# Kernel tuning notes

Hardware: AMD Instinct MI355X
Metric: run time of the kernel (lower is better)

The kernel has to match this reference:

```python
import jax, jax.numpy as jnp
import numpy as np

B, F, D, H = 16384, 39, 16, 2   # batch, fields, embed_dim, heads
VOCAB = 10000                    # per-field vocab
DH = D * H                       # attention output dim per layer (no head split)


def setup_inputs() -> dict:
    key = jax.random.key(0)
    ks = jax.random.split(key, 32)
    def n(k, shape, s=0.05):
        return jax.random.normal(k, shape, jnp.float32) * s
    inp = {"x": jax.random.randint(ks[0], (B, F), 0, VOCAB, dtype=jnp.int32)}
    inp["emb"] = n(ks[1], (F * VOCAB, D))
    idx = 2
    for i, din in enumerate([D, DH, DH]):  # layer0: 16->32, layers 1-2: 32->32
        for nm in ["wq", "wk", "wv", "wr"]:
            inp[f"{nm}{i}"] = n(ks[idx], (din, DH)); idx += 1
    prev = F * DH  # 1248 after flatten
    for i, u in enumerate([128, 64, 32, 1], 1):
        inp[f"w{i}"] = n(ks[idx], (prev, u)); idx += 1
        inp[f"b{i}"] = jnp.zeros((u,), jnp.float32)
        prev = u
    return inp


def reference(x, emb,
              wq0, wk0, wv0, wr0,
              wq1, wk1, wv1, wr1,
              wq2, wk2, wv2, wr2,
              w1, b1, w2, b2, w3, b3, w4, b4):
    offsets = jnp.arange(F, dtype=jnp.int32) * VOCAB
    e = emb[x + offsets]                                   # [B, F, D]
    for wq, wk, wv, wr in [(wq0, wk0, wv0, wr0),
                           (wq1, wk1, wv1, wr1),
                           (wq2, wk2, wv2, wr2)]:
        q = jnp.einsum('bfd,de->bfe', e, wq)               # [B, F, DH]
        k = jnp.einsum('bfd,de->bfe', e, wk)
        v = jnp.einsum('bfd,de->bfe', e, wv)
        att = jax.nn.softmax(jnp.einsum('bfe,bge->bfg', q, k), axis=-1)  # [B,F,F], no scaling
        out = jnp.einsum('bfg,bge->bfe', att, v) + jnp.einsum('bfd,de->bfe', e, wr)
        e = jax.nn.relu(out)
    h = e.reshape(B, F * DH)
    for w, b in [(w1, b1), (w2, b2), (w3, b3)]:
        h = jax.nn.relu(h @ w + b)
    return jax.nn.sigmoid(h @ w4 + b4)                     # [B, 1]
```

## Files before the change

kernel.cpp:

```cpp
#include <hip/hip_runtime.h>
#include <math.h>

#define NF   39
#define NB   16384
#define NVOC 10000

typedef unsigned short u16;
typedef unsigned int   u32;
typedef float f32x4 __attribute__((ext_vector_type(4)));
typedef short s16x8 __attribute__((ext_vector_type(8)));

#define E3_U16   20447232u
#define NSWZ     182272

__device__ __forceinline__ u32 bfadj(float x){
    u32 u = __float_as_uint(x);
    return u + 0x7fffu + ((u >> 16) & 1u);
}
__device__ __forceinline__ u32 pk2(float a, float b){
    return __builtin_amdgcn_perm(bfadj(a), bfadj(b), 0x03020706u);
}
__device__ __forceinline__ u16 f2bf(float f){ return (u16)(bfadj(f) >> 16); }

__device__ __forceinline__ void wave_sync(){
    asm volatile("s_waitcnt lgkmcnt(0)" ::: "memory");
}
__device__ __forceinline__ f32x4 mfma16(s16x8 a, s16x8 b, f32x4 c){
    return __builtin_amdgcn_mfma_f32_16x16x32_bf16(a, b, c, 0, 0, 0);
}
__device__ __forceinline__ void store4(u16* p, f32x4 v){
    *(uint2*)p = make_uint2(pk2(v[0], v[1]), pk2(v[2], v[3]));
}

__global__ void __launch_bounds__(256) swz_kernel(
    const float* __restrict__ wq0, const float* __restrict__ wk0,
    const float* __restrict__ wv0, const float* __restrict__ wr0,
    const float* __restrict__ wq1, const float* __restrict__ wk1,
    const float* __restrict__ wv1, const float* __restrict__ wr1,
    const float* __restrict__ wq2, const float* __restrict__ wk2,
    const float* __restrict__ wv2, const float* __restrict__ wr2,
    const float* __restrict__ w1, const float* __restrict__ w2,
    const float* __restrict__ w3, u16* __restrict__ ws)
{
    int gid = (int)blockIdx.x*256 + (int)threadIdx.x;
    if (gid >= NSWZ) return;
    int w    = gid & 511;
    int lane = w >> 3, j = w & 7;
    int n    = lane & 15, quad = lane >> 4;
    int kin  = quad*8 + j;
    float val;
    if (gid < 12288){
        int mat = gid >> 10;
        int nt  = (gid >> 9) & 1;
        const float* W;
        switch (mat){
            case 0: W = wq0; break; case 1: W = wk0; break;
            case 2: W = wv0; break; case 3: W = wr0; break;
            case 4: W = wq1; break; case 5: W = wk1; break;
            case 6: W = wv1; break; case 7: W = wr1; break;
            case 8: W = wq2; break; case 9: W = wk2; break;
            case 10: W = wv2; break; default: W = wr2; break;
        }
        int din = (mat < 4) ? 16 : 32;
        val = (kin < din) ? W[kin*32 + nt*16 + n] : 0.f;
    } else if (gid < 12288 + 159744){
        int tt = (gid - 12288) >> 9;
        int ks = tt >> 3, nt = tt & 7;
        val = w1[(ks*32 + kin)*128 + nt*16 + n];
    } else if (gid < 12288 + 159744 + 8192){
        int tt = (gid - (12288+159744)) >> 9;
        int ks = tt >> 2, nt = tt & 3;
        val = w2[(ks*32 + kin)*64 + nt*16 + n];
    } else {
        int tt = (gid - (12288+159744+8192)) >> 9;
        int ks = tt >> 1, nt = tt & 1;
        val = w3[(ks*32 + kin)*32 + nt*16 + n];
    }
    ws[E3_U16 + gid] = f2bf(val);
}

__global__ void __launch_bounds__(256, 3) attn_kernel(
    const int* __restrict__ x, const float* __restrict__ emb,
    u16* __restrict__ ws)
{
    __shared__ __align__(16) u16 lds[4*6656];
    const int tid  = (int)threadIdx.x;
    const int wid  = tid >> 6, lane = tid & 63;
    const int h    = lane >> 4, nl = lane & 15;
    const int r    = (int)blockIdx.x*4 + wid;

    u16* eBuf = lds + wid*6656;
    u16* kBuf = eBuf + 1536;
    u16* qBuf = kBuf + 1536;
    u16* vBuf = qBuf + 1536;
    u16* pBuf = kBuf;
    const u16* wmat = ws + E3_U16;
    const f32x4 z = {0.f, 0.f, 0.f, 0.f};
    const int A_off = nl*8 + (h>>1)*128 + (h&1)*4;

    f32x4 ci;
#pragma unroll
    for (int reg = 0; reg < 4; ++reg)
        ci[reg] = (h*4 + reg >= 7) ? -1e30f : 0.f;

    if (lane < 48){
        int f = lane, mt = f >> 4, fl = f & 15;
        u16* row = eBuf + mt*512 + fl*8;
        if (f < NF){
            const float4* ep = (const float4*)(emb + ((size_t)(x[r*NF + f] + f*NVOC))*16);
            float4 e0 = ep[0], e1 = ep[1], e2 = ep[2], e3 = ep[3];
            *(uint4*)(row)       = make_uint4(pk2(e0.x,e0.y), pk2(e0.z,e0.w),
                                              pk2(e1.x,e1.y), pk2(e1.z,e1.w));
            *(uint4*)(row + 128) = make_uint4(pk2(e2.x,e2.y), pk2(e2.z,e2.w),
                                              pk2(e3.x,e3.y), pk2(e3.z,e3.w));
        } else {
            *(uint4*)(row)       = make_uint4(0,0,0,0);
            *(uint4*)(row + 128) = make_uint4(0,0,0,0);
        }
        *(uint4*)(row + 256) = make_uint4(0,0,0,0);
        *(uint4*)(row + 384) = make_uint4(0,0,0,0);
    }
    wave_sync();

#pragma unroll 1
    for (int L = 0; L < 3; ++L){
        const u16* wB = wmat + L*4096;
        s16x8 bE[3];
#pragma unroll
        for (int nt = 0; nt < 3; ++nt)
            bE[nt] = *(const s16x8*)(eBuf + nt*512 + lane*8);

        {
            s16x8 a0 = *(const s16x8*)(wB + lane*8);
            s16x8 a1 = *(const s16x8*)(wB + 512 + lane*8);
#pragma unroll
            for (int nt = 0; nt < 3; ++nt){
                store4(qBuf + nt*512       + A_off, mfma16(a0, bE[nt], z));
                store4(qBuf + nt*512 + 256 + A_off, mfma16(a1, bE[nt], z));
            }
        }
        {
            s16x8 a0 = *(const s16x8*)(wB + 1024 + lane*8);
            s16x8 a1 = *(const s16x8*)(wB + 1536 + lane*8);
#pragma unroll
            for (int nt = 0; nt < 3; ++nt){
                store4(kBuf + nt*512       + A_off, mfma16(a0, bE[nt], z));
                store4(kBuf + nt*512 + 256 + A_off, mfma16(a1, bE[nt], z));
            }
        }
        {
            s16x8 b0 = *(const s16x8*)(wB + 2048 + lane*8);
            s16x8 b1 = *(const s16x8*)(wB + 2560 + lane*8);
#pragma unroll
            for (int mtg = 0; mtg < 3; ++mtg){
                int toff = (mtg>>1)*1024 + (mtg&1)*256;
                store4(vBuf + toff       + A_off, mfma16(bE[mtg], b0, z));
                store4(vBuf + toff + 512 + A_off, mfma16(bE[mtg], b1, z));
            }
            *(uint2*)(vBuf + 2*512 + 256 + lane*4) = make_uint2(0,0);
            *(uint2*)(vBuf + 3*512 + 256 + lane*4) = make_uint2(0,0);
        }
        f32x4 R[2][3];
        {
            s16x8 a0 = *(const s16x8*)(wB + 3072 + lane*8);
            s16x8 a1 = *(const s16x8*)(wB + 3584 + lane*8);
#pragma unroll
            for (int nt = 0; nt < 3; ++nt){
                R[0][nt] = mfma16(a0, bE[nt], z);
                R[1][nt] = mfma16(a1, bE[nt], z);
            }
        }
        wave_sync();

        f32x4 S[3][3];
        {
            s16x8 aK[3], bQ[3];
#pragma unroll
            for (int i = 0; i < 3; ++i){
                aK[i] = *(const s16x8*)(kBuf + i*512 + lane*8);
                bQ[i] = *(const s16x8*)(qBuf + i*512 + lane*8);
            }
#pragma unroll
            for (int mtg = 0; mtg < 3; ++mtg)
#pragma unroll
            for (int nt = 0; nt < 3; ++nt)
                S[mtg][nt] = mfma16(aK[mtg], bQ[nt], (mtg == 2) ? ci : z);
        }
        float inv[3];
#pragma unroll
        for (int nt = 0; nt < 3; ++nt){
            float t = 0.f;
#pragma unroll
            for (int mtg = 0; mtg < 3; ++mtg)
#pragma unroll
            for (int reg = 0; reg < 4; ++reg){
                S[mtg][nt][reg] = __expf(S[mtg][nt][reg]);
                t += S[mtg][nt][reg];
            }
            t += __shfl_xor(t, 16, 64);
            t += __shfl_xor(t, 32, 64);
            inv[nt] = 1.0f / t;
        }
#pragma unroll
        for (int mtg = 0; mtg < 3; ++mtg)
#pragma unroll
        for (int nt = 0; nt < 3; ++nt){
            f32x4 p;
#pragma unroll
            for (int reg = 0; reg < 4; ++reg) p[reg] = S[mtg][nt][reg]*inv[nt];
            store4(pBuf + ((mtg>>1)*3 + nt)*512 + (mtg&1)*256 + A_off, p);
        }
        wave_sync();

        s16x8 aV[2][2], bP[2][3];
#pragma unroll
        for (int ks = 0; ks < 2; ++ks){
#pragma unroll
            for (int emt = 0; emt < 2; ++emt)
                aV[ks][emt] = *(const s16x8*)(vBuf + (ks*2+emt)*512 + lane*8);
#pragma unroll
            for (int nt = 0; nt < 3; ++nt)
                bP[ks][nt] = *(const s16x8*)(pBuf + (ks*3+nt)*512 + lane*8);
        }
        if (L < 2){
#pragma unroll
            for (int emt = 0; emt < 2; ++emt)
#pragma unroll
            for (int nt = 0; nt < 3; ++nt){
                f32x4 o = mfma16(aV[1][emt], bP[1][nt],
                         mfma16(aV[0][emt], bP[0][nt], z));
                float m = (nt < 2 || nl < 7) ? 1.f : 0.f;
#pragma unroll
                for (int reg = 0; reg < 4; ++reg)
                    o[reg] = fmaxf(o[reg] + R[emt][nt][reg], 0.f) * m;
                store4(eBuf + nt*512 + emt*256 + A_off, o);
            }
        } else {
            int st = r >> 4, sm = r & 15;
            u32 base = (u32)(st*39)*512u + (u32)(sm*8 + (h>>1)*128 + (h&1)*4);
#pragma unroll
            for (int emt = 0; emt < 2; ++emt)
#pragma unroll
            for (int nt = 0; nt < 3; ++nt){
                f32x4 o = mfma16(aV[1][emt], bP[1][nt],
                         mfma16(aV[0][emt], bP[0][nt], z));
#pragma unroll
                for (int reg = 0; reg < 4; ++reg)
                    o[reg] = fmaxf(o[reg] + R[emt][nt][reg], 0.f);
                int f = nt*16 + nl;
                if (f < NF)
                    *(uint2*)(ws + base + (u32)f*512u + emt*256) =
                        make_uint2(pk2(o[0], o[1]), pk2(o[2], o[3]));
            }
        }
        wave_sync();
    }
}

__global__ void __launch_bounds__(256, 4) mlp_kernel(
    const float* __restrict__ b1, const float* __restrict__ b2,
    const float* __restrict__ b3, const float* __restrict__ w4,
    const float* __restrict__ b4, const u16* __restrict__ ws,
    float* __restrict__ out)
{
    __shared__ __align__(16) u16 h1t[2048];
    __shared__ __align__(16) u16 h2t[1024];
    __shared__ float part[32];
    const int tid = (int)threadIdx.x;
    const int w   = tid >> 6, lane = tid & 63;
    const int h   = lane >> 4, nl = lane & 15;
    const int st  = (int)blockIdx.x;
    const int A_off = nl*8 + (h>>1)*128 + (h&1)*4;

    const u16* w1b = ws + E3_U16 + 12288u;
    const u16* w2b = w1b + 159744u;
    const u16* w3b = w2b + 8192u;
    const f32x4 z = {0.f,0.f,0.f,0.f};

    f32x4 acc[2] = {z, z};
#pragma unroll 2
    for (int ks = 0; ks < 39; ++ks){
        s16x8 aE = *(const s16x8*)(ws + (u32)(st*39 + ks)*512u + lane*8);
#pragma unroll
        for (int t = 0; t < 2; ++t){
            s16x8 aW = *(const s16x8*)(w1b + (ks*8 + 2*w + t)*512 + lane*8);
            acc[t] = mfma16(aW, aE, acc[t]);
        }
    }
#pragma unroll
    for (int t = 0; t < 2; ++t){
        float4 bv = *(const float4*)(b1 + (2*w + t)*16 + h*4);
        f32x4 v;
        v[0] = fmaxf(acc[t][0] + bv.x, 0.f);
        v[1] = fmaxf(acc[t][1] + bv.y, 0.f);
        v[2] = fmaxf(acc[t][2] + bv.z, 0.f);
        v[3] = fmaxf(acc[t][3] + bv.w, 0.f);
        store4(h1t + w*512 + t*256 + A_off, v);
    }
    __syncthreads();

    {
        f32x4 a2 = z;
#pragma unroll
        for (int ks = 0; ks < 4; ++ks){
            s16x8 aW = *(const s16x8*)(w2b + (ks*4 + w)*512 + lane*8);
            s16x8 bH = *(const s16x8*)(h1t + ks*512 + lane*8);
            a2 = mfma16(aW, bH, a2);
        }
        float4 bv = *(const float4*)(b2 + w*16 + h*4);
        f32x4 v;
        v[0] = fmaxf(a2[0] + bv.x, 0.f);
        v[1] = fmaxf(a2[1] + bv.y, 0.f);
        v[2] = fmaxf(a2[2] + bv.z, 0.f);
        v[3] = fmaxf(a2[3] + bv.w, 0.f);
        store4(h2t + (w>>1)*512 + (w&1)*256 + A_off, v);
    }
    __syncthreads();

    if (w < 2){
        f32x4 a3 = z;
#pragma unroll
        for (int ks = 0; ks < 2; ++ks){
            s16x8 aW = *(const s16x8*)(w3b + (ks*2 + w)*512 + lane*8);
            s16x8 bH = *(const s16x8*)(h2t + ks*512 + lane*8);
            a3 = mfma16(aW, bH, a3);
        }
        float4 b3v = *(const float4*)(b3 + w*16 + h*4);
        float4 w4v = *(const float4*)(w4 + w*16 + h*4);
        float t = fmaxf(a3[0] + b3v.x, 0.f)*w4v.x
                + fmaxf(a3[1] + b3v.y, 0.f)*w4v.y
                + fmaxf(a3[2] + b3v.z, 0.f)*w4v.z
                + fmaxf(a3[3] + b3v.w, 0.f)*w4v.w;
        t += __shfl_xor(t, 16, 64);
        t += __shfl_xor(t, 32, 64);
        if (h == 0) part[w*16 + nl] = t;
    }
    __syncthreads();
    if (tid < 16){
        float zz = part[tid] + part[16 + tid] + b4[0];
        out[st*16 + tid] = 1.f/(1.f + __expf(-zz));
    }
}

extern "C" void kernel_launch(void* const* d_in, const int* in_sizes, int n_in,
                              void* d_out, int out_size, void* d_ws, size_t ws_size,
                              hipStream_t stream)
{
    (void)in_sizes; (void)n_in; (void)ws_size; (void)out_size;
    const int*   x   = (const int*)d_in[0];
    const float* emb = (const float*)d_in[1];
    u16* ws = (u16*)d_ws;

    swz_kernel<<<(NSWZ+255)/256, 256, 0, stream>>>(
        (const float*)d_in[2],  (const float*)d_in[3],  (const float*)d_in[4],  (const float*)d_in[5],
        (const float*)d_in[6],  (const float*)d_in[7],  (const float*)d_in[8],  (const float*)d_in[9],
        (const float*)d_in[10], (const float*)d_in[11], (const float*)d_in[12], (const float*)d_in[13],
        (const float*)d_in[14], (const float*)d_in[16], (const float*)d_in[18], ws);

    attn_kernel<<<NB/4, 256, 0, stream>>>(x, emb, ws);

    mlp_kernel<<<NB/16, 256, 0, stream>>>(
        (const float*)d_in[15], (const float*)d_in[17], (const float*)d_in[19],
        (const float*)d_in[20], (const float*)d_in[21], ws, (float*)d_out);
}
```

Before: 195.3 us.

## Split MLP layer-1 K across waves, defer softmax normalization, use hardware bf16 pack

```diff
diff --git a/kernel.cpp b/kernel.cpp
--- a/kernel.cpp
+++ b/kernel.cpp
@@ -18,7 +18,12 @@
     return u + 0x7fffu + ((u >> 16) & 1u);
 }
 __device__ __forceinline__ u32 pk2(float a, float b){
+#if __has_builtin(__builtin_amdgcn_cvt_pk_bf16_f32)
+    auto t = __builtin_amdgcn_cvt_pk_bf16_f32(a, b);
+    u32 r; __builtin_memcpy(&r, &t, 4); return r;
+#else
     return __builtin_amdgcn_perm(bfadj(a), bfadj(b), 0x03020706u);
+#endif
 }
 __device__ __forceinline__ u16 f2bf(float f){ return (u16)(bfadj(f) >> 16); }
 
@@ -204,12 +209,8 @@
 #pragma unroll
         for (int mtg = 0; mtg < 3; ++mtg)
 #pragma unroll
-        for (int nt = 0; nt < 3; ++nt){
-            f32x4 p;
-#pragma unroll
-            for (int reg = 0; reg < 4; ++reg) p[reg] = S[mtg][nt][reg]*inv[nt];
-            store4(pBuf + ((mtg>>1)*3 + nt)*512 + (mtg&1)*256 + A_off, p);
-        }
+        for (int nt = 0; nt < 3; ++nt)
+            store4(pBuf + ((mtg>>1)*3 + nt)*512 + (mtg&1)*256 + A_off, S[mtg][nt]);
         wave_sync();
 
         s16x8 aV[2][2], bP[2][3];
@@ -232,7 +233,7 @@
                 float m = (nt < 2 || nl < 7) ? 1.f : 0.f;
 #pragma unroll
                 for (int reg = 0; reg < 4; ++reg)
-                    o[reg] = fmaxf(o[reg] + R[emt][nt][reg], 0.f) * m;
+                    o[reg] = fmaxf(fmaf(o[reg], inv[nt], R[emt][nt][reg]), 0.f) * m;
                 store4(eBuf + nt*512 + emt*256 + A_off, o);
             }
         } else {
@@ -246,7 +247,7 @@
                          mfma16(aV[0][emt], bP[0][nt], z));
 #pragma unroll
                 for (int reg = 0; reg < 4; ++reg)
-                    o[reg] = fmaxf(o[reg] + R[emt][nt][reg], 0.f);
+                    o[reg] = fmaxf(fmaf(o[reg], inv[nt], R[emt][nt][reg]), 0.f);
                 int f = nt*16 + nl;
                 if (f < NF)
                     *(uint2*)(ws + base + (u32)f*512u + emt*256) =
@@ -263,6 +264,7 @@
     const float* __restrict__ b4, const u16* __restrict__ ws,
     float* __restrict__ out)
 {
+    __shared__ __align__(16) float red[8192];
     __shared__ __align__(16) u16 h1t[2048];
     __shared__ __align__(16) u16 h2t[1024];
     __shared__ float part[32];
@@ -277,25 +279,40 @@
     const u16* w3b = w2b + 8192u;
     const f32x4 z = {0.f,0.f,0.f,0.f};
 
-    f32x4 acc[2] = {z, z};
-#pragma unroll 2
-    for (int ks = 0; ks < 39; ++ks){
+    f32x4 acc[8];
+#pragma unroll
+    for (int nt = 0; nt < 8; ++nt) acc[nt] = z;
+#pragma unroll 1
+    for (int ks = w; ks < 39; ks += 4){
         s16x8 aE = *(const s16x8*)(ws + (u32)(st*39 + ks)*512u + lane*8);
 #pragma unroll
-        for (int t = 0; t < 2; ++t){
-            s16x8 aW = *(const s16x8*)(w1b + (ks*8 + 2*w + t)*512 + lane*8);
-            acc[t] = mfma16(aW, aE, acc[t]);
-        }
-    }
+        for (int nt = 0; nt < 8; ++nt){
+            s16x8 aW = *(const s16x8*)(w1b + (ks*8 + nt)*512 + lane*8);
+            acc[nt] = mfma16(aW, aE, acc[nt]);
+        }
+    }
+#pragma unroll
+    for (int nt = 0; nt < 8; ++nt)
+        *(f32x4*)(red + (w*8 + nt)*256 + lane*4) = acc[nt];
+    __syncthreads();
+
 #pragma unroll
     for (int t = 0; t < 2; ++t){
-        float4 bv = *(const float4*)(b1 + (2*w + t)*16 + h*4);
+        int ft = 2*w + t;
+        f32x4 s = *(const f32x4*)(red + (0*8 + ft)*256 + lane*4);
+#pragma unroll
+        for (int p = 1; p < 4; ++p){
+            f32x4 q = *(const f32x4*)(red + (p*8 + ft)*256 + lane*4);
+#pragma unroll
+            for (int reg = 0; reg < 4; ++reg) s[reg] += q[reg];
+        }
+        float4 bv = *(const float4*)(b1 + ft*16 + h*4);
         f32x4 v;
-        v[0] = fmaxf(acc[t][0] + bv.x, 0.f);
-        v[1] = fmaxf(acc[t][1] + bv.y, 0.f);
-        v[2] = fmaxf(acc[t][2] + bv.z, 0.f);
-        v[3] = fmaxf(acc[t][3] + bv.w, 0.f);
-        store4(h1t + w*512 + t*256 + A_off, v);
+        v[0] = fmaxf(s[0] + bv.x, 0.f);
+        v[1] = fmaxf(s[1] + bv.y, 0.f);
+        v[2] = fmaxf(s[2] + bv.z, 0.f);
+        v[3] = fmaxf(s[3] + bv.w, 0.f);
+        store4(h1t + ft*256 + A_off, v);
     }
     __syncthreads();
 
```

After: 192.1 us. About the same (-1.6%).
